# Kernel tuning notes

Hardware: AMD Instinct MI355X
Metric: run time of the kernel (lower is better)

## Reference

```python
import jax, jax.numpy as jnp
import numpy as np

BS = 64; T = 96; C = 16; IN = 16; H = 256; NH = 8; DH = H // NH
NCLS = 4; L = T + NCLS; LAYERS = 4; GDEP = 2; EPS = 1e-5


def _ln(x, g, b):
    m = x.mean(-1, keepdims=True)
    v = ((x - m) ** 2).mean(-1, keepdims=True)
    return (x - m) / jnp.sqrt(v + EPS) * g + b


def _mask():
    # causal upper-triangular -inf mask; last NCLS rows (cls tokens) attend everywhere
    m = jnp.where(jnp.triu(jnp.ones((L, L), jnp.float32), 1) > 0, -jnp.inf, 0.0)
    return m.at[-NCLS:].set(0.0)


def _enc(h, mask, Wqkv, bqkv, Wo, bo, W1, b1, W2, b2, g1, be1, g2, be2):
    # post-norm TransformerEncoderLayer (torch default), dropout=0
    B = h.shape[0]
    qkv = h @ Wqkv.T + bqkv
    q, k, v = jnp.split(qkv, 3, axis=-1)
    sp = lambda t: t.reshape(B, L, NH, DH).transpose(0, 2, 1, 3)
    q, k, v = sp(q), sp(k), sp(v)
    s = jnp.einsum('bhqd,bhkd->bhqk', q, k) / np.float32(np.sqrt(DH)) + mask
    a = jax.nn.softmax(s, axis=-1)
    o = jnp.einsum('bhqk,bhkd->bhqd', a, v).transpose(0, 2, 1, 3).reshape(B, L, H)
    h = _ln(h + o @ Wo.T + bo, g1, be1)
    ff = jax.nn.relu(h @ W1.T + b1) @ W2.T + b2
    return _ln(h + ff, g2, be2)


def _mixprop(x, g, Wm, bm):
    # x: (bs, H, C, NCLS); MTGNN mixprop with alpha=0
    adj = g + jnp.eye(C, dtype=g.dtype)
    a = adj / adj.sum(1, keepdims=True)
    h = x
    outs = [x]
    for _ in range(GDEP):
        h = jnp.einsum('ncwl,vw->ncvl', h, a)
        outs.append(h)
    ho = jnp.concatenate(outs, axis=1)  # (bs, (GDEP+1)*H, C, NCLS)
    return jnp.einsum('ncwl,oc->nowl', ho, Wm) + bm[None, :, None, None]


def _forward(x, Wfc, bfc, cls_token, pos_emb, emb1, emb2, Wl1, bl1, Wl2, bl2,
             Wqkv, bqkv, Wo, bo, W1, b1, W2, b2, ln1g, ln1b, ln2g, ln2b,
             Wmlp, bmlp, Wd1, bd1, Wd2, bd2):
    bs = x.shape[0]
    h = x @ Wfc.T + bfc                                      # (bs,T,C,H)
    h = jnp.concatenate([h, jnp.broadcast_to(cls_token, (bs, NCLS, C, H))], axis=1)
    h = h + pos_emb[None]                                    # (bs,L,C,H)
    h = jnp.swapaxes(h, 1, 2).reshape(bs * C, L, H)
    mask = _mask()
    # graph_constructor (alpha=1)
    m1 = jnp.tanh(emb1 @ Wl1.T + bl1)
    m2 = jnp.tanh(emb2 @ Wl2.T + bl2)
    g = jax.nn.relu(jnp.tanh(m1 @ m2.T - m2 @ m1.T))         # (C,C)
    h = _enc(h, mask, Wqkv[0], bqkv[0], Wo[0], bo[0], W1[0], b1[0], W2[0], b2[0],
             ln1g[0], ln1b[0], ln2g[0], ln2b[0])
    for l in range(1, LAYERS):
        cls = h[:, -NCLS:].reshape(bs, C, NCLS, H).transpose(0, 3, 1, 2)  # (bs,H,C,NCLS)
        cls = _mixprop(cls, g, Wmlp[l - 1], bmlp[l - 1])
        cls = cls.transpose(0, 2, 3, 1).reshape(bs * C, NCLS, H)
        h = jnp.concatenate([h[:, :-NCLS], cls], axis=1)
        h = _enc(h, mask, Wqkv[l], bqkv[l], Wo[l], bo[l], W1[l], b1[l], W2[l], b2[l],
                 ln1g[l], ln1b[l], ln2g[l], ln2b[l])
    z = jnp.tanh(h[:, -NCLS:].reshape(bs, C * NCLS * H))
    z = jax.nn.gelu(z @ Wd1.T + bd1, approximate=False) @ Wd2.T + bd2
    return z[:, 0]


def setup_inputs() -> dict:
    key = jax.random.key(0)
    ks = iter(jax.random.split(key, 64))
    rn = lambda *s: jax.random.normal(next(ks), s, dtype=jnp.float32) * 0.05
    d = {}
    d['x'] = jax.random.normal(next(ks), (BS, T, C, IN), dtype=jnp.float32)
    d['p'] = jnp.zeros((BS,), jnp.float32)
    d['y'] = jnp.zeros((BS,), jnp.float32)
    d['Wfc'] = rn(H, IN); d['bfc'] = jnp.zeros((H,), jnp.float32)
    d['cls_token'] = rn(1, NCLS, C, H) * 20.0  # torch randn scale ~1
    d['pos_emb'] = rn(NCLS + T, C, H) * 20.0
    d['emb1'] = rn(C, H); d['emb2'] = rn(C, H)
    d['Wl1'] = rn(H, H); d['bl1'] = jnp.zeros((H,), jnp.float32)
    d['Wl2'] = rn(H, H); d['bl2'] = jnp.zeros((H,), jnp.float32)
    d['Wqkv'] = rn(LAYERS, 3 * H, H); d['bqkv'] = jnp.zeros((LAYERS, 3 * H), jnp.float32)
    d['Wo'] = rn(LAYERS, H, H); d['bo'] = jnp.zeros((LAYERS, H), jnp.float32)
    d['W1'] = rn(LAYERS, 4 * H, H); d['b1'] = jnp.zeros((LAYERS, 4 * H), jnp.float32)
    d['W2'] = rn(LAYERS, H, 4 * H); d['b2'] = jnp.zeros((LAYERS, H), jnp.float32)
    d['ln1g'] = jnp.ones((LAYERS, H), jnp.float32); d['ln1b'] = jnp.zeros((LAYERS, H), jnp.float32)
    d['ln2g'] = jnp.ones((LAYERS, H), jnp.float32); d['ln2b'] = jnp.zeros((LAYERS, H), jnp.float32)
    d['Wmlp'] = rn(LAYERS - 1, H, (GDEP + 1) * H); d['bmlp'] = jnp.zeros((LAYERS - 1, H), jnp.float32)
    d['Wd1'] = rn(H, NCLS * C * H); d['bd1'] = jnp.zeros((H,), jnp.float32)
    d['Wd2'] = rn(1, H); d['bd2'] = jnp.zeros((1,), jnp.float32)
    return d


def reference(x, p, y, Wfc, bfc, cls_token, pos_emb, emb1, emb2, Wl1, bl1, Wl2, bl2,
              Wqkv, bqkv, Wo, bo, W1, b1, W2, b2, ln1g, ln1b, ln2g, ln2b,
              Wmlp, bmlp, Wd1, bd1, Wd2, bd2):
    # p, y are unused by the original forward (kept for signature parity)
    return _forward(x, Wfc, bfc, cls_token, pos_emb, emb1, emb2, Wl1, bl1, Wl2, bl2,
                    Wqkv, bqkv, Wo, bo, W1, b1, W2, b2, ln1g, ln1b, ln2g, ln2b,
                    Wmlp, bmlp, Wd1, bd1, Wd2, bd2)
```

## Files before the change

kernel.cpp:

```cpp
#include <hip/hip_runtime.h>
#include <hip/hip_bf16.h>
#include <math.h>

typedef unsigned short u16;
typedef unsigned int   u32;
typedef __attribute__((ext_vector_type(8))) short short8;
typedef __attribute__((ext_vector_type(4))) float f32x4;

#define BSZ   64
#define TT    96
#define CCH   16
#define INDIM 16
#define HD    256
#define NHEAD 8
#define DHEAD 32
#define NCLS  4
#define LSEQ  100
#define NLAY  4
#define EPSV  1e-5f
#define BSEQ  (BSZ*CCH)
#define MTOK  (BSEQ*LSEQ)

__device__ __forceinline__ float bf2f(u16 x){ return __uint_as_float(((u32)x)<<16); }
__device__ __forceinline__ u16 f2bf(float f){
    u32 u = __float_as_uint(f);
    u32 r = (u + 0x7fffu + ((u>>16)&1u)) >> 16;
    return (u16)r;
}
__device__ __forceinline__ float lo16(u32 r){ return __uint_as_float(r<<16); }
__device__ __forceinline__ float hi16(u32 r){ return __uint_as_float(r&0xffff0000u); }

__device__ __forceinline__ void gload_lds16(const u16* g, u16* l){
    __builtin_amdgcn_global_load_lds(
        (const __attribute__((address_space(1))) unsigned int*)g,
        (__attribute__((address_space(3))) unsigned int*)l, 16, 0, 0);
}

__global__ __launch_bounds__(256)
void k_cvt(const float* __restrict__ src, u16* __restrict__ dst, int n)
{
    for (int i = blockIdx.x*256 + threadIdx.x; i < n; i += gridDim.x*256)
        dst[i] = f2bf(src[i]);
}

__global__ __launch_bounds__(256)
void k_embed(const float* __restrict__ x, const float* __restrict__ Wfc,
             const float* __restrict__ bfc, const float* __restrict__ cls,
             const float* __restrict__ pos, u16* __restrict__ h)
{
    int s = blockIdx.x;
    int n = s >> 4, c = s & 15;
    int hc = threadIdx.x;
    float wr[INDIM];
    #pragma unroll
    for (int i=0;i<INDIM;i++) wr[i] = Wfc[hc*INDIM + i];
    float bb = bfc[hc];
    for (int l=0; l<TT; l++){
        const float* xr = x + (size_t)((n*TT + l)*CCH + c)*INDIM;
        float acc = bb;
        #pragma unroll
        for (int i=0;i<INDIM;i++) acc += xr[i]*wr[i];
        acc += pos[(size_t)(l*CCH + c)*HD + hc];
        h[((size_t)s*LSEQ + l)*HD + hc] = f2bf(acc);
    }
    #pragma unroll
    for (int l=TT; l<LSEQ; l++){
        float v = cls[(size_t)((l-TT)*CCH + c)*HD + hc]
                + pos[(size_t)(l*CCH + c)*HD + hc];
        h[((size_t)s*LSEQ + l)*HD + hc] = f2bf(v);
    }
}

__global__ __launch_bounds__(256)
void k_graph_m(const float* __restrict__ emb, const float* __restrict__ Wl,
               const float* __restrict__ bl, float* __restrict__ m)
{
    int r = blockIdx.x, o = threadIdx.x;
    __shared__ float e[HD];
    e[o] = emb[r*HD + o];
    __syncthreads();
    const float* w = Wl + (size_t)o*HD;
    float acc = bl[o];
    for (int k=0;k<HD;k++) acc += e[k]*w[k];
    m[r*HD + o] = tanhf(acc);
}

__global__ __launch_bounds__(256)
void k_graph_a(const float* __restrict__ m1, const float* __restrict__ m2,
               float* __restrict__ a)
{
    int t = threadIdx.x; int v = t >> 4, w = t & 15;
    __shared__ float adj[16][17];
    float s1=0.f, s2=0.f;
    for (int k=0;k<HD;k++){
        s1 += m1[v*HD+k]*m2[w*HD+k];
        s2 += m2[v*HD+k]*m1[w*HD+k];
    }
    float g = tanhf(s1 - s2); g = g > 0.f ? g : 0.f;
    adj[v][w] = g + (v==w ? 1.f : 0.f);
    __syncthreads();
    float rs = 0.f;
    #pragma unroll
    for (int j=0;j<16;j++) rs += adj[v][j];
    a[t] = adj[v][w] / rs;
}

__global__ __launch_bounds__(256)
void k_gemmA(const u16* __restrict__ A, int lda,
             const u16* __restrict__ W, const float* __restrict__ bias,
             u16* __restrict__ C, int ldc, int K, int relu, int scat)
{
    __shared__ u16 As0[128*32], As1[128*32];
    __shared__ u16 Ws0[128*32], Ws1[128*32];
    int t = threadIdx.x;
    int lane = t & 63, w = t >> 6;
    int wm = (w & 1)*64, wn = (w >> 1)*64;
    int fr = lane & 15, quad = lane >> 4;
    size_t mb = (size_t)blockIdx.x * 128;
    int nb = blockIdx.y * 128;
    int srow = lane >> 2;
    int sslot = lane & 3;

    f32x4 acc[4][4] = {};
    for (int k0 = 0; k0 < K; k0 += 64){
        __syncthreads();
        #pragma unroll
        for (int i=0;i<2;i++){
            int r = w*32 + i*16 + srow;
            int cw = sslot ^ ((r>>1)&3);
            gload_lds16(&A[(mb + r)*(size_t)lda + k0      + cw*8], &As0[(w*32 + i*16)*32]);
            gload_lds16(&A[(mb + r)*(size_t)lda + k0 + 32 + cw*8], &As1[(w*32 + i*16)*32]);
            gload_lds16(&W[(size_t)(nb + r)*K   + k0      + cw*8], &Ws0[(w*32 + i*16)*32]);
            gload_lds16(&W[(size_t)(nb + r)*K   + k0 + 32 + cw*8], &Ws1[(w*32 + i*16)*32]);
        }
        __syncthreads();
        short8 af0[4], af1[4], bf0[4], bf1[4];
        #pragma unroll
        for (int mt=0; mt<4; mt++){
            int r = wm + mt*16 + fr;
            int sw = (quad ^ ((r>>1)&3)) << 3;
            af0[mt] = *(const short8*)&As0[r*32 + sw];
            af1[mt] = *(const short8*)&As1[r*32 + sw];
        }
        #pragma unroll
        for (int nt=0; nt<4; nt++){
            int r = wn + nt*16 + fr;
            int sw = (quad ^ ((r>>1)&3)) << 3;
            bf0[nt] = *(const short8*)&Ws0[r*32 + sw];
            bf1[nt] = *(const short8*)&Ws1[r*32 + sw];
        }
        #pragma unroll
        for (int mt=0; mt<4; mt++)
            #pragma unroll
            for (int nt=0; nt<4; nt++){
                acc[mt][nt] = __builtin_amdgcn_mfma_f32_16x16x32_bf16(
                    af0[mt], bf0[nt], acc[mt][nt], 0, 0, 0);
                acc[mt][nt] = __builtin_amdgcn_mfma_f32_16x16x32_bf16(
                    af1[mt], bf1[nt], acc[mt][nt], 0, 0, 0);
            }
    }
    float bb[4];
    #pragma unroll
    for (int nt=0; nt<4; nt++) bb[nt] = bias[nb + wn + nt*16 + fr];
    #pragma unroll
    for (int mt=0; mt<4; mt++){
        #pragma unroll
        for (int nt=0; nt<4; nt++){
            #pragma unroll
            for (int r=0; r<4; r++){
                float v = acc[mt][nt][r] + bb[nt];
                if (relu) v = v > 0.f ? v : 0.f;
                size_t rg = mb + wm + mt*16 + quad*4 + r;
                if (scat) rg = (rg >> 2)*LSEQ + TT + (rg & 3);
                C[rg*(size_t)ldc + nb + wn + nt*16 + fr] = f2bf(v);
            }
        }
    }
}

__global__ __launch_bounds__(256)
void k_gemmC(const u16* __restrict__ A, int lda, int K,
             const u16* __restrict__ W, const float* __restrict__ bias,
             u16* __restrict__ h, const float* __restrict__ gam,
             const float* __restrict__ bet, size_t row0)
{
    __shared__ u16 As0[64*32], As1[64*32];
    __shared__ u16 Ws0[256*32], Ws1[256*32];
    int t = threadIdx.x;
    int lane = t & 63, w = t >> 6;
    int fr = lane & 15, quad = lane >> 4;
    size_t mb = (size_t)blockIdx.x * 64;
    int srow = lane >> 2, sslot = lane & 3;

    f32x4 acc[16] = {};
    for (int k0 = 0; k0 < K; k0 += 64){
        __syncthreads();
        {
            int r = w*16 + srow;
            int cw = sslot ^ ((r>>1)&3);
            gload_lds16(&A[(mb + r)*(size_t)lda + k0      + cw*8], &As0[(w*16)*32]);
            gload_lds16(&A[(mb + r)*(size_t)lda + k0 + 32 + cw*8], &As1[(w*16)*32]);
        }
        #pragma unroll
        for (int i=0;i<4;i++){
            int r = w*64 + i*16 + srow;
            int cw = sslot ^ ((r>>1)&3);
            gload_lds16(&W[(size_t)r*K + k0      + cw*8], &Ws0[(w*64 + i*16)*32]);
            gload_lds16(&W[(size_t)r*K + k0 + 32 + cw*8], &Ws1[(w*64 + i*16)*32]);
        }
        __syncthreads();
        int ra = w*16 + fr;
        int swa = (quad ^ ((ra>>1)&3)) << 3;
        short8 a0 = *(const short8*)&As0[ra*32 + swa];
        short8 a1 = *(const short8*)&As1[ra*32 + swa];
        #pragma unroll
        for (int nt=0; nt<16; nt++){
            int rb = nt*16 + fr;
            int swb = (quad ^ ((rb>>1)&3)) << 3;
            short8 b0 = *(const short8*)&Ws0[rb*32 + swb];
            short8 b1 = *(const short8*)&Ws1[rb*32 + swb];
            acc[nt] = __builtin_amdgcn_mfma_f32_16x16x32_bf16(a0, b0, acc[nt], 0,0,0);
            acc[nt] = __builtin_amdgcn_mfma_f32_16x16x32_bf16(a1, b1, acc[nt], 0,0,0);
        }
    }
    float bb[16], gg[16], be[16];
    #pragma unroll
    for (int nt=0; nt<16; nt++){
        int col = nt*16 + fr;
        bb[nt] = bias[col]; gg[nt] = gam[col]; be[nt] = bet[col];
    }
    #pragma unroll
    for (int r=0; r<4; r++){
        size_t row = row0 + mb + w*16 + quad*4 + r;
        float v[16];
        float s = 0.f;
        #pragma unroll
        for (int nt=0; nt<16; nt++){
            v[nt] = acc[nt][r] + bb[nt] + bf2f(h[row*HD + nt*16 + fr]);
            s += v[nt];
        }
        s += __shfl_xor(s, 1, 64); s += __shfl_xor(s, 2, 64);
        s += __shfl_xor(s, 4, 64); s += __shfl_xor(s, 8, 64);
        float mean = s * (1.f/256.f);
        float vv = 0.f;
        #pragma unroll
        for (int nt=0; nt<16; nt++){ float d = v[nt]-mean; vv += d*d; }
        vv += __shfl_xor(vv, 1, 64); vv += __shfl_xor(vv, 2, 64);
        vv += __shfl_xor(vv, 4, 64); vv += __shfl_xor(vv, 8, 64);
        float inv = rsqrtf(vv*(1.f/256.f) + EPSV);
        #pragma unroll
        for (int nt=0; nt<16; nt++)
            h[row*HD + nt*16 + fr] = f2bf((v[nt]-mean)*inv*gg[nt] + be[nt]);
    }
}

#define KS_STR 40
#define VT_STR 136
#define PL_STR 136
__global__ __launch_bounds__(256)
void k_attn(u16* __restrict__ qkv)
{
    __shared__ u16 smem[26368];
    int t = threadIdx.x;
    int w = t >> 6, lane = t & 63;
    int fr = lane & 15, quad = lane >> 4;
    int p = t >> 7, t2 = t & 127;
    u16* Ks = smem + p*4480;
    u16* Vt = smem + 8960 + p*4352;
    u16* Pl = smem + 17664 + w*2176;

    {
        int gp = blockIdx.x*2 + p;
        size_t base = (size_t)(gp >> 3)*LSEQ*768 + (gp & 7)*32;
        for (int idx = t2; idx < 1792; idx += 128){
            int key = idx >> 4, d2 = (idx & 15) << 1;
            u32 kv = (key < LSEQ) ? *(const u32*)&qkv[base + (size_t)key*768 + 256 + d2] : 0u;
            *(u32*)&Ks[key*KS_STR + d2] = kv;
        }
        for (int idx = t2; idx < 2048; idx += 128){
            int key = idx >> 4, d2 = (idx & 15) << 1;
            u32 vv = (key < LSEQ) ? *(const u32*)&qkv[base + (size_t)key*768 + 512 + d2] : 0u;
            Vt[ d2   *VT_STR + key] = (u16)(vv & 0xffffu);
            Vt[(d2+1)*VT_STR + key] = (u16)(vv >> 16);
        }
    }
    __syncthreads();

    int wp = w >> 1;
    int gp = blockIdx.x*2 + wp;
    size_t base = (size_t)(gp >> 3)*LSEQ*768 + (gp & 7)*32;
    u16* Ksw = smem + wp*4480;
    u16* Vtw = smem + 8960 + wp*4352;

    short8 kf[7];
    #pragma unroll
    for (int nt=0; nt<7; nt++)
        kf[nt] = *(const short8*)&Ksw[(nt*16 + fr)*KS_STR + quad*8];
    short8 vfr[4][2];
    #pragma unroll
    for (int ks=0; ks<4; ks++)
        #pragma unroll
        for (int nt=0; nt<2; nt++)
            vfr[ks][nt] = *(const short8*)&Vtw[(nt*16 + fr)*VT_STR + ks*32 + quad*8];

    const float scale = 0.17677669529663687f;
    int smask = (w & 1) ? 0x34 : 0x4B;
    #pragma unroll
    for (int st = 0; st < 7; ++st){
        if (!((smask >> st) & 1)) continue;
        const int ntile = (st == 6) ? 7 : (st + 1);
        const int nks   = (st == 6) ? 4 : (st/2 + 1);
        int q = st*16 + fr;
        short8 qf = {};
        if (q < LSEQ) qf = *(const short8*)&qkv[base + (size_t)q*768 + quad*8];
        f32x4 S[7];
        #pragma unroll
        for (int nt=0; nt<7; nt++){
            if (nt >= ntile) continue;
            f32x4 z = {};
            S[nt] = __builtin_amdgcn_mfma_f32_16x16x32_bf16(qf, kf[nt], z, 0,0,0);
        }
        float mx[4] = {-1e30f,-1e30f,-1e30f,-1e30f};
        #pragma unroll
        for (int r=0;r<4;r++){
            int qr = st*16 + quad*4 + r;
            int jmax = (qr < TT) ? qr : (LSEQ-1);
            #pragma unroll
            for (int nt=0;nt<7;nt++){
                if (nt >= ntile) continue;
                int j = nt*16 + fr;
                float s = (j <= jmax) ? S[nt][r]*scale : -1e30f;
                S[nt][r] = s;
                mx[r] = fmaxf(mx[r], s);
            }
        }
        #pragma unroll
        for (int r=0;r<4;r++){
            #pragma unroll
            for (int m=1;m<16;m<<=1) mx[r] = fmaxf(mx[r], __shfl_xor(mx[r], m, 64));
        }
        float l4[4] = {0.f,0.f,0.f,0.f};
        #pragma unroll
        for (int r=0;r<4;r++){
            #pragma unroll
            for (int nt=0;nt<7;nt++){
                if (nt >= ntile) continue;
                float pv = __expf(S[nt][r] - mx[r]);
                S[nt][r] = pv;
                l4[r] += pv;
            }
        }
        #pragma unroll
        for (int r=0;r<4;r++){
            #pragma unroll
            for (int m=1;m<16;m<<=1) l4[r] += __shfl_xor(l4[r], m, 64);
        }
        #pragma unroll
        for (int nt=0;nt<7;nt++){
            if (nt >= ntile) continue;
            #pragma unroll
            for (int r=0;r<4;r++){
                u16 hb = f2bf(S[nt][r]);
                Pl[(quad*4+r)*PL_STR + nt*16 + fr] = hb;
                S[nt][r] -= bf2f(hb);
            }
        }
        if (ntile*16 < nks*32){
            #pragma unroll
            for (int r=0;r<4;r++)
                Pl[(quad*4+r)*PL_STR + ntile*16 + fr] = 0;
        }
        __builtin_amdgcn_s_waitcnt(0);
        f32x4 D[2] = {};
        #pragma unroll
        for (int ks=0; ks<4; ks++){
            if (ks >= nks) continue;
            short8 pf = *(const short8*)&Pl[fr*PL_STR + ks*32 + quad*8];
            #pragma unroll
            for (int nt=0; nt<2; nt++)
                D[nt] = __builtin_amdgcn_mfma_f32_16x16x32_bf16(pf, vfr[ks][nt], D[nt], 0,0,0);
        }
        __builtin_amdgcn_s_waitcnt(0);
        #pragma unroll
        for (int nt=0;nt<7;nt++){
            if (nt >= ntile) continue;
            #pragma unroll
            for (int r=0;r<4;r++)
                Pl[(quad*4+r)*PL_STR + nt*16 + fr] = f2bf(S[nt][r]);
        }
        __builtin_amdgcn_s_waitcnt(0);
        #pragma unroll
        for (int ks=0; ks<4; ks++){
            if (ks >= nks) continue;
            short8 pf = *(const short8*)&Pl[fr*PL_STR + ks*32 + quad*8];
            #pragma unroll
            for (int nt=0; nt<2; nt++)
                D[nt] = __builtin_amdgcn_mfma_f32_16x16x32_bf16(pf, vfr[ks][nt], D[nt], 0,0,0);
        }
        #pragma unroll
        for (int r=0;r<4;r++){
            int qr = st*16 + quad*4 + r;
            if (qr < LSEQ){
                float inv = 1.f / l4[r];
                #pragma unroll
                for (int nt=0; nt<2; nt++)
                    qkv[base + (size_t)qr*768 + nt*16 + fr] = f2bf(D[nt][r]*inv);
            }
        }
        __builtin_amdgcn_s_waitcnt(0);
    }
}

__global__ __launch_bounds__(256)
void k_mixprep(const u16* __restrict__ h, const float* __restrict__ a,
               u16* __restrict__ amid)
{
    int n = blockIdx.x >> 2, tt = blockIdx.x & 3;
    __shared__ float xs[256][17], h1s[256][17], h2s[256][17];
    __shared__ float as[16][17];
    int t = threadIdx.x;
    as[t>>4][t&15] = a[t];
    for (int idx=t; idx<4096; idx+=256){
        int w = idx >> 8, hc = idx & 255;
        xs[hc][w] = bf2f(h[((size_t)(n*16 + w)*LSEQ + TT + tt)*HD + hc]);
    }
    __syncthreads();
    for (int idx=t; idx<4096; idx+=256){
        int v = idx & 15, hc = idx >> 4;
        float acc = 0.f;
        #pragma unroll
        for (int w=0;w<16;w++) acc += as[v][w]*xs[hc][w];
        h1s[hc][v] = acc;
    }
    __syncthreads();
    for (int idx=t; idx<4096; idx+=256){
        int v = idx & 15, hc = idx >> 4;
        float acc = 0.f;
        #pragma unroll
        for (int w=0;w<16;w++) acc += as[v][w]*h1s[hc][w];
        h2s[hc][v] = acc;
    }
    __syncthreads();
    int hc = t;
    #pragma unroll
    for (int w=0;w<16;w++){
        size_t row = (size_t)((n*16 + w)*4 + tt);
        amid[row*768 +       hc] = f2bf(xs[hc][w]);
        amid[row*768 + 256 + hc] = f2bf(h1s[hc][w]);
        amid[row*768 + 512 + hc] = f2bf(h2s[hc][w]);
    }
}

__global__ __launch_bounds__(256)
void k_z(const u16* __restrict__ h, u16* __restrict__ z)
{
    int bid = blockIdx.x, t = threadIdx.x;
    #pragma unroll
    for (int tc=0;tc<4;tc++)
        z[((size_t)bid*4 + tc)*HD + t] = f2bf(tanhf(bf2f(h[((size_t)bid*LSEQ + TT + tc)*HD + t])));
}

__global__ __launch_bounds__(256)
void k_head1p(const u16* __restrict__ z, const float* __restrict__ Wd1,
              float* __restrict__ d1p)
{
    __shared__ float zch[64][137];
    __shared__ float wt[16][137];
    int t = threadIdx.x;
    int col = t & 15, rgrp = t >> 4;
    int ob = blockIdx.x * 16;
    int kb = blockIdx.y;
    float acc[4] = {0.f,0.f,0.f,0.f};
    for (int kc=0; kc<1024; kc+=128){
        int base_k = kb*1024 + kc;
        #pragma unroll
        for (int jj=0; jj<16; jj++){
            int idx = t + jj*256;
            int n = idx >> 6, k2 = (idx & 63) << 1;
            u32 r = *(const u32*)&z[(size_t)n*16384 + base_k + k2];
            zch[n][k2] = lo16(r); zch[n][k2+1] = hi16(r);
        }
        #pragma unroll
        for (int jj=0; jj<2; jj++){
            int idx = t + jj*256;
            int r = idx >> 5, k4 = (idx & 31) << 2;
            float4 w4 = *(const float4*)&Wd1[(size_t)(ob + r)*16384 + base_k + k4];
            wt[r][k4] = w4.x; wt[r][k4+1] = w4.y; wt[r][k4+2] = w4.z; wt[r][k4+3] = w4.w;
        }
        __syncthreads();
        for (int k=0;k<128;k++){
            float wv = wt[col][k];
            #pragma unroll
            for (int u=0;u<4;u++) acc[u] += zch[rgrp + 16*u][k]*wv;
        }
        __syncthreads();
    }
    #pragma unroll
    for (int u=0;u<4;u++)
        d1p[(size_t)(kb*64 + rgrp + 16*u)*HD + ob + col] = acc[u];
}

__global__ __launch_bounds__(256)
void k_headf(const float* __restrict__ d1p, const float* __restrict__ bd1,
             const float* __restrict__ Wd2, const float* __restrict__ bd2,
             float* __restrict__ out)
{
    __shared__ float red[4];
    int n = blockIdx.x, c = threadIdx.x;
    float s = 0.f;
    #pragma unroll
    for (int kb=0; kb<16; kb++) s += d1p[(size_t)(kb*64 + n)*HD + c];
    float xx = s + bd1[c];
    float ge = 0.5f*xx*(1.f + erff(xx*0.70710678118654752f));
    float p = ge * Wd2[c];
    #pragma unroll
    for (int m=1;m<64;m<<=1) p += __shfl_xor(p, m, 64);
    if ((c & 63) == 0) red[c >> 6] = p;
    __syncthreads();
    if (c == 0) out[n] = red[0]+red[1]+red[2]+red[3] + bd2[0];
}

extern "C" void kernel_launch(void* const* d_in, const int* in_sizes, int n_in,
                              void* d_out, int out_size, void* d_ws, size_t ws_size,
                              hipStream_t stream)
{
    const float* x    = (const float*)d_in[0];
    const float* Wfc  = (const float*)d_in[3];
    const float* bfc  = (const float*)d_in[4];
    const float* cls  = (const float*)d_in[5];
    const float* pos  = (const float*)d_in[6];
    const float* emb1 = (const float*)d_in[7];
    const float* emb2 = (const float*)d_in[8];
    const float* Wl1  = (const float*)d_in[9];
    const float* bl1  = (const float*)d_in[10];
    const float* Wl2  = (const float*)d_in[11];
    const float* bl2  = (const float*)d_in[12];
    const float* Wqkv = (const float*)d_in[13];
    const float* bqkv = (const float*)d_in[14];
    const float* Wo   = (const float*)d_in[15];
    const float* bo   = (const float*)d_in[16];
    const float* W1   = (const float*)d_in[17];
    const float* b1   = (const float*)d_in[18];
    const float* W2   = (const float*)d_in[19];
    const float* b2   = (const float*)d_in[20];
    const float* ln1g = (const float*)d_in[21];
    const float* ln1b = (const float*)d_in[22];
    const float* ln2g = (const float*)d_in[23];
    const float* ln2b = (const float*)d_in[24];
    const float* Wmlp = (const float*)d_in[25];
    const float* bmlp = (const float*)d_in[26];
    const float* Wd1  = (const float*)d_in[27];
    const float* bd1  = (const float*)d_in[28];
    const float* Wd2  = (const float*)d_in[29];
    const float* bd2  = (const float*)d_in[30];

    int NCH = 8;
    {
        const size_t fixed = 63145088 + (1<<20);
        if      (fixed + (size_t)MTOK    *2560 <= ws_size) NCH = 1;
        else if (fixed + (size_t)(MTOK/2)*2560 <= ws_size) NCH = 2;
        else if (fixed + (size_t)(MTOK/4)*2560 <= ws_size) NCH = 4;
    }
    const int RCH = MTOK / NCH;
    const int SCH = BSEQ / NCH;

    u16* h    = (u16*)d_ws;
    u16* buf  = h    + (size_t)MTOK*HD;
    u16* buf2 = buf  + (size_t)RCH*1024;
    u16* wq   = buf2 + (size_t)RCH*256;
    u16* wo   = wq   + (size_t)4*768*256;
    u16* w1   = wo   + (size_t)4*256*256;
    u16* w2   = w1   + (size_t)4*1024*256;
    u16* wmb  = w2   + (size_t)4*256*1024;
    u16* zb   = wmb  + (size_t)3*256*768;
    float* fp = (float*)(zb + (size_t)BSZ*16384);
    float* m1  = fp;
    float* m2  = m1 + CCH*HD;
    float* an  = m2 + CCH*HD;
    float* d1p = an + CCH*CCH;

    k_cvt<<<512, 256, 0, stream>>>(Wqkv, wq, 4*768*256);
    k_cvt<<<256, 256, 0, stream>>>(Wo,   wo, 4*256*256);
    k_cvt<<<512, 256, 0, stream>>>(W1,   w1, 4*1024*256);
    k_cvt<<<512, 256, 0, stream>>>(W2,   w2, 4*256*1024);
    k_cvt<<<256, 256, 0, stream>>>(Wmlp, wmb, 3*256*768);

    k_embed<<<BSEQ, 256, 0, stream>>>(x, Wfc, bfc, cls, pos, h);
    k_graph_m<<<16, 256, 0, stream>>>(emb1, Wl1, bl1, m1);
    k_graph_m<<<16, 256, 0, stream>>>(emb2, Wl2, bl2, m2);
    k_graph_a<<<1, 256, 0, stream>>>(m1, m2, an);

    for (int l=0; l<NLAY; l++){
        if (l > 0){
            k_mixprep<<<BSZ*NCLS, 256, 0, stream>>>(h, an, buf);
            k_gemmA<<<dim3(4096/128, 256/128), 256, 0, stream>>>(
                buf, 768, wmb + (size_t)(l-1)*256*768, bmlp + (size_t)(l-1)*HD,
                h, HD, 768, 0, 1);
        }

        for (int c=0; c<NCH; c++){
            size_t row0 = (size_t)c * RCH;
            k_gemmA<<<dim3(RCH/128, 768/128), 256, 0, stream>>>(
                h + row0*HD, HD, wq + (size_t)l*768*256, bqkv + (size_t)l*768,
                buf, 768, HD, 0, 0);
            k_attn<<<SCH*NHEAD/2, 256, 0, stream>>>(buf);
            k_gemmC<<<RCH/64, 256, 0, stream>>>(
                buf, 768, HD, wo + (size_t)l*256*256, bo + (size_t)l*HD,
                h, ln1g + (size_t)l*HD, ln1b + (size_t)l*HD, row0);
            k_gemmA<<<dim3(RCH/128, 1024/128), 256, 0, stream>>>(
                h + row0*HD, HD, w1 + (size_t)l*1024*256, b1 + (size_t)l*1024,
                buf, 1024, HD, 1, 0);
            k_gemmC<<<RCH/64, 256, 0, stream>>>(
                buf, 1024, 1024, w2 + (size_t)l*256*1024, b2 + (size_t)l*HD,
                h, ln2g + (size_t)l*HD, ln2b + (size_t)l*HD, row0);
        }
    }

    k_z<<<BSZ*CCH, 256, 0, stream>>>(h, zb);
    k_head1p<<<dim3(16, 16), 256, 0, stream>>>(zb, Wd1, d1p);
    k_headf<<<BSZ, 256, 0, stream>>>(d1p, bd1, Wd2, bd2, (float*)d_out);
}
```

Baseline: 2.244 ms.

## Split output columns across waves in residual+LayerNorm GEMM with cross-wave LDS reduction

Reorganizes k_gemmC so each wave computes a 64x64 tile (4x4 MFMA fragments over all 64 rows and a quarter of the columns) instead of 16 rows by all 256 columns. This cuts per-wave LDS fragment loads (4 A + 4 B per half instead of 1 A + 16 B) and improves operand reuse in registers. The LayerNorm epilogue now needs row statistics across waves, so it adds two shared-memory reduction passes and extra barriers.

```diff
diff --git a/kernel.cpp b/kernel.cpp
--- a/kernel.cpp
+++ b/kernel.cpp
@@ -192,7 +192,7 @@
     size_t mb = (size_t)blockIdx.x * 64;
     int srow = lane >> 2, sslot = lane & 3;
 
-    f32x4 acc[16] = {};
+    f32x4 acc[4][4] = {};
     for (int k0 = 0; k0 < K; k0 += 64){
         __syncthreads();
         {
@@ -209,49 +209,104 @@
             gload_lds16(&W[(size_t)r*K + k0 + 32 + cw*8], &Ws1[(w*64 + i*16)*32]);
         }
         __syncthreads();
-        int ra = w*16 + fr;
-        int swa = (quad ^ ((ra>>1)&3)) << 3;
-        short8 a0 = *(const short8*)&As0[ra*32 + swa];
-        short8 a1 = *(const short8*)&As1[ra*32 + swa];
-        #pragma unroll
-        for (int nt=0; nt<16; nt++){
-            int rb = nt*16 + fr;
+        short8 af0[4], af1[4], bf0[4], bf1[4];
+        #pragma unroll
+        for (int mt=0; mt<4; mt++){
+            int ra = mt*16 + fr;
+            int swa = (quad ^ ((ra>>1)&3)) << 3;
+            af0[mt] = *(const short8*)&As0[ra*32 + swa];
+            af1[mt] = *(const short8*)&As1[ra*32 + swa];
+        }
+        #pragma unroll
+        for (int nt=0; nt<4; nt++){
+            int rb = w*64 + nt*16 + fr;
             int swb = (quad ^ ((rb>>1)&3)) << 3;
-            short8 b0 = *(const short8*)&Ws0[rb*32 + swb];
-            short8 b1 = *(const short8*)&Ws1[rb*32 + swb];
-            acc[nt] = __builtin_amdgcn_mfma_f32_16x16x32_bf16(a0, b0, acc[nt], 0,0,0);
-            acc[nt] = __builtin_amdgcn_mfma_f32_16x16x32_bf16(a1, b1, acc[nt], 0,0,0);
-        }
-    }
-    float bb[16], gg[16], be[16];
-    #pragma unroll
-    for (int nt=0; nt<16; nt++){
-        int col = nt*16 + fr;
+            bf0[nt] = *(const short8*)&Ws0[rb*32 + swb];
+            bf1[nt] = *(const short8*)&Ws1[rb*32 + swb];
+        }
+        #pragma unroll
+        for (int mt=0; mt<4; mt++)
+            #pragma unroll
+            for (int nt=0; nt<4; nt++){
+                acc[mt][nt] = __builtin_amdgcn_mfma_f32_16x16x32_bf16(
+                    af0[mt], bf0[nt], acc[mt][nt], 0, 0, 0);
+                acc[mt][nt] = __builtin_amdgcn_mfma_f32_16x16x32_bf16(
+                    af1[mt], bf1[nt], acc[mt][nt], 0, 0, 0);
+            }
+    }
+
+    float bb[4], gg[4], be[4];
+    #pragma unroll
+    for (int nt=0; nt<4; nt++){
+        int col = w*64 + nt*16 + fr;
         bb[nt] = bias[col]; gg[nt] = gam[col]; be[nt] = bet[col];
     }
     #pragma unroll
-    for (int r=0; r<4; r++){
-        size_t row = row0 + mb + w*16 + quad*4 + r;
-        float v[16];
-        float s = 0.f;
-        #pragma unroll
-        for (int nt=0; nt<16; nt++){
-            v[nt] = acc[nt][r] + bb[nt] + bf2f(h[row*HD + nt*16 + fr]);
-            s += v[nt];
-        }
-        s += __shfl_xor(s, 1, 64); s += __shfl_xor(s, 2, 64);
-        s += __shfl_xor(s, 4, 64); s += __shfl_xor(s, 8, 64);
-        float mean = s * (1.f/256.f);
-        float vv = 0.f;
-        #pragma unroll
-        for (int nt=0; nt<16; nt++){ float d = v[nt]-mean; vv += d*d; }
-        vv += __shfl_xor(vv, 1, 64); vv += __shfl_xor(vv, 2, 64);
-        vv += __shfl_xor(vv, 4, 64); vv += __shfl_xor(vv, 8, 64);
-        float inv = rsqrtf(vv*(1.f/256.f) + EPSV);
-        #pragma unroll
-        for (int nt=0; nt<16; nt++)
-            h[row*HD + nt*16 + fr] = f2bf((v[nt]-mean)*inv*gg[nt] + be[nt]);
-    }
+    for (int mt=0; mt<4; mt++){
+        #pragma unroll
+        for (int r=0; r<4; r++){
+            size_t row = row0 + mb + mt*16 + quad*4 + r;
+            #pragma unroll
+            for (int nt=0; nt<4; nt++)
+                acc[mt][nt][r] += bb[nt] + bf2f(h[row*HD + w*64 + nt*16 + fr]);
+        }
+    }
+    __syncthreads();
+    float* red  = (float*)As0;
+    float* red2 = (float*)As1;
+    float ps[4][4];
+    #pragma unroll
+    for (int mt=0; mt<4; mt++)
+        #pragma unroll
+        for (int r=0; r<4; r++){
+            float s = acc[mt][0][r] + acc[mt][1][r] + acc[mt][2][r] + acc[mt][3][r];
+            s += __shfl_xor(s,1,64); s += __shfl_xor(s,2,64);
+            s += __shfl_xor(s,4,64); s += __shfl_xor(s,8,64);
+            ps[mt][r] = s;
+        }
+    if (fr == 0){
+        #pragma unroll
+        for (int mt=0; mt<4; mt++)
+            #pragma unroll
+            for (int r=0; r<4; r++)
+                red[w*64 + mt*16 + quad*4 + r] = ps[mt][r];
+    }
+    __syncthreads();
+    float mean[4][4];
+    #pragma unroll
+    for (int mt=0; mt<4; mt++)
+        #pragma unroll
+        for (int r=0; r<4; r++){
+            int rl = mt*16 + quad*4 + r;
+            mean[mt][r] = (red[rl] + red[64+rl] + red[128+rl] + red[192+rl]) * (1.f/256.f);
+            float s = 0.f;
+            #pragma unroll
+            for (int nt=0; nt<4; nt++){ float d = acc[mt][nt][r] - mean[mt][r]; s += d*d; }
+            s += __shfl_xor(s,1,64); s += __shfl_xor(s,2,64);
+            s += __shfl_xor(s,4,64); s += __shfl_xor(s,8,64);
+            ps[mt][r] = s;
+        }
+    if (fr == 0){
+        #pragma unroll
+        for (int mt=0; mt<4; mt++)
+            #pragma unroll
+            for (int r=0; r<4; r++)
+                red2[w*64 + mt*16 + quad*4 + r] = ps[mt][r];
+    }
+    __syncthreads();
+    #pragma unroll
+    for (int mt=0; mt<4; mt++)
+        #pragma unroll
+        for (int r=0; r<4; r++){
+            int rl = mt*16 + quad*4 + r;
+            float inv = rsqrtf((red2[rl] + red2[64+rl] + red2[128+rl] + red2[192+rl])
+                               * (1.f/256.f) + EPSV);
+            size_t row = row0 + mb + rl;
+            #pragma unroll
+            for (int nt=0; nt<4; nt++)
+                h[row*HD + w*64 + nt*16 + fr] =
+                    f2bf((acc[mt][nt][r] - mean[mt][r]) * inv * gg[nt] + be[nt]);
+        }
 }
 
 #define KS_STR 40
```

New measurement: 2.352 ms. +4.8%, slower.
